# Kernel tuning notes

Measured on AMD Instinct MI355X. Metric: run time of the kernel, lower is better.

## Reference

```python
import jax, jax.numpy as jnp
import numpy as np

B, S, D = 8, 1024, 768
H, DQK, DV = 12, 64, 64
DHEAD = 2 * DQK + DV  # 192, interleaved per-head qkv layout
DOUT = 768


def setup_inputs() -> dict:
    key = jax.random.key(0)
    k1, k2, k3, k4 = jax.random.split(key, 4)
    x = jax.random.normal(k1, (B, S, D), dtype=jnp.float32)
    w_qkv = jax.random.normal(k2, (D, H * DHEAD), dtype=jnp.float32) * (D ** -0.5)
    w_out = jax.random.normal(k3, (H * DV, DOUT), dtype=jnp.float32) * ((H * DV) ** -0.5)
    b_out = jax.random.normal(k4, (DOUT,), dtype=jnp.float32) * 0.02
    return {"x": x, "w_qkv": w_qkv, "w_out": w_out, "b_out": b_out}


def reference(x, w_qkv, w_out, b_out):
    scale = DQK ** -0.5
    # Interleaved per-head layout: [B,S,H,DHEAD] then split into q|k|v blocks.
    qkv = (x @ w_qkv).reshape(B, S, H, DHEAD)
    q = qkv[..., :DQK]                 # [B,S,H,DQK]
    k = qkv[..., DQK:2 * DQK]          # [B,S,H,DQK]
    v = qkv[..., 2 * DQK:]             # [B,S,H,DV]
    scores = jnp.einsum("bshd,bthd->bhst", q, k) * scale  # [B,H,S,S]
    attn = jax.nn.softmax(scores, axis=-1)
    out = jnp.einsum("bhst,bthd->bshd", attn, v)           # [B,S,H,DV]
    out = out.reshape(B, S, H * DV)
    return out @ w_out + b_out
```

## Files before the change

kernel.cpp:

```cpp
#include <hip/hip_runtime.h>
#include <hip/hip_bf16.h>
#include <cstdint>

namespace {

constexpr int kB = 8;
constexpr int kS = 1024;
constexpr int kD = 768;
constexpr int kH = 12;
constexpr int kDH = 192;
constexpr int kNQ = kH * kDH;
constexpr int kM = kB * kS;
constexpr int kDO = 768;

using f32x4 = __attribute__((ext_vector_type(4))) float;
using s16x8 = __attribute__((ext_vector_type(8))) short;
using u16x8 = __attribute__((ext_vector_type(8))) unsigned short;

__device__ __forceinline__ unsigned short f2bf(float f) {
  union { float f; uint32_t u; } v; v.f = f;
  uint32_t u = v.u;
  u += 0x7FFFu + ((u >> 16) & 1u);
  return (unsigned short)(u >> 16);
}

__device__ __forceinline__ void load_lds16(const void* g, void* l) {
  __builtin_amdgcn_global_load_lds((__attribute__((address_space(1))) void*)g,
                                   (__attribute__((address_space(3))) void*)l,
                                   16, 0, 0);
}


__global__ __launch_bounds__(256) void cvt_x_kernel(const float* __restrict__ in,
                                                    unsigned short* __restrict__ out) {
  int i = (blockIdx.x * 256 + threadIdx.x) * 8;
  float4 a = *(const float4*)(in + i);
  float4 b = *(const float4*)(in + i + 4);
  u16x8 o;
  o[0] = f2bf(a.x); o[1] = f2bf(a.y); o[2] = f2bf(a.z); o[3] = f2bf(a.w);
  o[4] = f2bf(b.x); o[5] = f2bf(b.y); o[6] = f2bf(b.z); o[7] = f2bf(b.w);
  *(u16x8*)(out + i) = o;
}

__global__ __launch_bounds__(256) void cvt_transpose_kernel(const float* __restrict__ w,
                                                            unsigned short* __restrict__ wt,
                                                            int K, int N) {
  __shared__ float tile[32][33];
  int k0 = blockIdx.x * 32, n0 = blockIdx.y * 32;
  int tx = threadIdx.x & 31, ty = threadIdx.x >> 5;
  #pragma unroll
  for (int r = 0; r < 32; r += 8)
    tile[ty + r][tx] = w[(size_t)(k0 + ty + r) * N + n0 + tx];
  __syncthreads();
  #pragma unroll
  for (int r = 0; r < 32; r += 8)
    wt[(size_t)(n0 + ty + r) * K + k0 + tx] = f2bf(tile[tx][ty + r]);
}

template <int MODE>
__global__ __launch_bounds__(256, 2) void gemm_bt_kernel(
    const unsigned short* __restrict__ A,
    const unsigned short* __restrict__ Bt,
    void* __restrict__ Cout,
    const float* __restrict__ bias,
    int M, int N, int K) {
  __shared__ alignas(16) unsigned short Al[128 * 64];
  __shared__ alignas(16) unsigned short Bl[128 * 64];
  const int nT = N >> 7;
  const int tm = blockIdx.x / nT, tn = blockIdx.x % nT;
  const int tid = threadIdx.x;
  const int w = tid >> 6, l = tid & 63;
  const int wr = w >> 1, wc = w & 1;
  const int la = l & 15, g = l >> 4;
  const int sr = l >> 3, sc = l & 7;

  f32x4 acc[4][4] = {};
  const unsigned short* Ag = A + (size_t)(tm * 128) * K;
  const unsigned short* Bg = Bt + (size_t)(tn * 128) * K;

  for (int k0 = 0; k0 < K; k0 += 64) {
    #pragma unroll
    for (int j = 0; j < 4; ++j) {
      int row = w * 32 + j * 8 + sr;
      load_lds16(Ag + (size_t)row * K + k0 + sc * 8, &Al[row * 64 + sc * 8]);
      load_lds16(Bg + (size_t)row * K + k0 + sc * 8, &Bl[row * 64 + sc * 8]);
    }
    __syncthreads();
    #pragma unroll
    for (int kk = 0; kk < 2; ++kk) {
      s16x8 af[4], bfv[4];
      #pragma unroll
      for (int i = 0; i < 4; ++i)
        af[i] = *(const s16x8*)&Al[(wr * 64 + i * 16 + la) * 64 + kk * 32 + g * 8];
      #pragma unroll
      for (int j = 0; j < 4; ++j)
        bfv[j] = *(const s16x8*)&Bl[(wc * 64 + j * 16 + la) * 64 + kk * 32 + g * 8];
      #pragma unroll
      for (int i = 0; i < 4; ++i)
        #pragma unroll
        for (int j = 0; j < 4; ++j)
          acc[i][j] = __builtin_amdgcn_mfma_f32_16x16x32_bf16(af[i], bfv[j], acc[i][j], 0, 0, 0);
    }
    __syncthreads();
  }

  #pragma unroll
  for (int i = 0; i < 4; ++i) {
    int row0 = tm * 128 + wr * 64 + i * 16 + g * 4;
    #pragma unroll
    for (int j = 0; j < 4; ++j) {
      int col = tn * 128 + wc * 64 + j * 16 + la;
      if (MODE == 0) {
        unsigned short* C = (unsigned short*)Cout;
        float sc2 = ((col % 192) < 64) ? 0.125f : 1.0f;
        #pragma unroll
        for (int r = 0; r < 4; ++r)
          C[(size_t)(row0 + r) * N + col] = f2bf(acc[i][j][r] * sc2);
      } else {
        float* C = (float*)Cout;
        float bv = bias[col];
        #pragma unroll
        for (int r = 0; r < 4; ++r)
          C[(size_t)(row0 + r) * N + col] = acc[i][j][r] + bv;
      }
    }
  }
}

__global__ __launch_bounds__(256, 2) void attn_kernel(
    const unsigned short* __restrict__ qkv,
    unsigned short* __restrict__ Ab) {
  const int qb = blockIdx.x, h = blockIdx.y, b = blockIdx.z;
  const int tid = threadIdx.x;
  const int w = tid >> 6, l = tid & 63;
  const int la = l & 15, g = l >> 4;

  __shared__ alignas(16) unsigned short Ql[64 * 64];
  __shared__ alignas(16) unsigned short Kl[64 * 64];
  __shared__ alignas(16) unsigned short Vt[64 * 64];
  __shared__ alignas(16) unsigned short Pl[64 * 64];

  const size_t base_bs = (size_t)b * kS;
  const size_t qrow0 = base_bs + (size_t)qb * 64;

  {
    int row = tid >> 2, c0 = (tid & 3) * 2;
    const unsigned short* src = qkv + (qrow0 + row) * kNQ + h * kDH + c0 * 8;
    u16x8 v0 = *(const u16x8*)(src);
    u16x8 v1 = *(const u16x8*)(src + 8);
    int x = row & 7;
    *(u16x8*)&Ql[row * 64 + ((c0 ^ x) * 8)] = v0;
    *(u16x8*)&Ql[row * 64 + (((c0 + 1) ^ x) * 8)] = v1;
  }
  s16x8 qf[2];
  {
    int row = w * 16 + la, x = row & 7;
    #pragma unroll
    for (int ks = 0; ks < 2; ++ks)
      qf[ks] = *(const s16x8*)&Ql[row * 64 + (((ks * 4 + g) ^ x) * 8)];
  }

  float mrow[4], lrow[4];
  #pragma unroll
  for (int r = 0; r < 4; ++r) { mrow[r] = -1e30f; lrow[r] = 0.f; }
  f32x4 oacc[4] = {};
  const float LOG2E = 1.44269504088896340736f;

  for (int kt = 0; kt < 16; ++kt) {
    __syncthreads();
    {
      int row = tid >> 2, c0 = (tid & 3) * 2;
      const unsigned short* srcK = qkv + (base_bs + kt * 64 + row) * kNQ + h * kDH + 64 + c0 * 8;
      u16x8 k0v = *(const u16x8*)(srcK);
      u16x8 k1v = *(const u16x8*)(srcK + 8);
      int x = row & 7;
      *(u16x8*)&Kl[row * 64 + ((c0 ^ x) * 8)] = k0v;
      *(u16x8*)&Kl[row * 64 + (((c0 + 1) ^ x) * 8)] = k1v;

      int tv = tid >> 2, d0 = (tid & 3) * 16;
      const unsigned short* srcV = qkv + (base_bs + kt * 64 + tv) * kNQ + h * kDH + 128 + d0;
      u16x8 v0 = *(const u16x8*)(srcV);
      u16x8 v1 = *(const u16x8*)(srcV + 8);
      #pragma unroll
      for (int e = 0; e < 8; ++e) {
        int d1 = d0 + e;
        int x1 = (d1 & 7) ^ ((d1 >> 3) & 7);
        Vt[d1 * 64 + (tv ^ (x1 << 3))] = (unsigned short)v0[e];
        int d2 = d0 + 8 + e;
        int x2 = (d2 & 7) ^ ((d2 >> 3) & 7);
        Vt[d2 * 64 + (tv ^ (x2 << 3))] = (unsigned short)v1[e];
      }
    }
    __syncthreads();

    f32x4 sacc[4] = {};
    #pragma unroll
    for (int ks = 0; ks < 2; ++ks) {
      #pragma unroll
      for (int tb = 0; tb < 4; ++tb) {
        int row = tb * 16 + la, x = row & 7;
        s16x8 kf = *(const s16x8*)&Kl[row * 64 + (((ks * 4 + g) ^ x) * 8)];
        sacc[tb] = __builtin_amdgcn_mfma_f32_16x16x32_bf16(qf[ks], kf, sacc[tb], 0, 0, 0);
      }
    }

    #pragma unroll
    for (int r = 0; r < 4; ++r) {
      float m = fmaxf(fmaxf(sacc[0][r], sacc[1][r]), fmaxf(sacc[2][r], sacc[3][r]));
      #pragma unroll
      for (int msk = 1; msk < 16; msk <<= 1) m = fmaxf(m, __shfl_xor(m, msk, 64));
      float mnew = fmaxf(mrow[r], m);
      float corr = exp2f((mrow[r] - mnew) * LOG2E);
      mrow[r] = mnew;
      float s = 0.f;
      #pragma unroll
      for (int tb = 0; tb < 4; ++tb) {
        float p = exp2f((sacc[tb][r] - mnew) * LOG2E);
        sacc[tb][r] = p;
        s += p;
      }
      #pragma unroll
      for (int msk = 1; msk < 16; msk <<= 1) s += __shfl_xor(s, msk, 64);
      lrow[r] = lrow[r] * corr + s;
      #pragma unroll
      for (int db = 0; db < 4; ++db) oacc[db][r] *= corr;
    }

    #pragma unroll
    for (int r = 0; r < 4; ++r) {
      int prow = w * 16 + g * 4 + r, x = prow & 7;
      #pragma unroll
      for (int tb = 0; tb < 4; ++tb) {
        int col = tb * 16 + la;
        Pl[prow * 64 + (col ^ (x << 3))] = f2bf(sacc[tb][r]);
      }
    }

    #pragma unroll
    for (int ks = 0; ks < 2; ++ks) {
      int prow = w * 16 + la, x = prow & 7;
      s16x8 pf = *(const s16x8*)&Pl[prow * 64 + (((ks * 4 + g) ^ x) * 8)];
      #pragma unroll
      for (int db = 0; db < 4; ++db) {
        int drow = db * 16 + la;
        int xv = (drow & 7) ^ ((drow >> 3) & 7);
        s16x8 vf = *(const s16x8*)&Vt[drow * 64 + (((ks * 4 + g) ^ xv) * 8)];
        oacc[db] = __builtin_amdgcn_mfma_f32_16x16x32_bf16(pf, vf, oacc[db], 0, 0, 0);
      }
    }
  }

  #pragma unroll
  for (int db = 0; db < 4; ++db) {
    #pragma unroll
    for (int r = 0; r < 4; ++r) {
      int row = w * 16 + g * 4 + r;
      Ab[(qrow0 + row) * (size_t)(kH * 64) + h * 64 + db * 16 + la] =
          f2bf(oacc[db][r] / lrow[r]);
    }
  }
}

}

extern "C" void kernel_launch(void* const* d_in, const int* in_sizes, int n_in,
                              void* d_out, int out_size, void* d_ws, size_t ws_size,
                              hipStream_t stream) {
  (void)in_sizes; (void)n_in; (void)out_size; (void)ws_size;
  const float* x = (const float*)d_in[0];
  const float* w_qkv = (const float*)d_in[1];
  const float* w_out = (const float*)d_in[2];
  const float* b_out = (const float*)d_in[3];

  unsigned short* Xb = (unsigned short*)d_ws;
  unsigned short* WqT = Xb + (size_t)kM * kD;
  unsigned short* WoT = WqT + (size_t)kNQ * kD;
  unsigned short* QKV = WoT + (size_t)kDO * kDO;
  unsigned short* Ab = QKV + (size_t)kM * kNQ;

  cvt_x_kernel<<<dim3((kM * kD) / (256 * 8)), dim3(256), 0, stream>>>(x, Xb);
  cvt_transpose_kernel<<<dim3(kD / 32, kNQ / 32), dim3(256), 0, stream>>>(w_qkv, WqT, kD, kNQ);
  cvt_transpose_kernel<<<dim3(kDO / 32, kDO / 32), dim3(256), 0, stream>>>(w_out, WoT, kDO, kDO);

  gemm_bt_kernel<0><<<dim3((kM / 128) * (kNQ / 128)), dim3(256), 0, stream>>>(
      Xb, WqT, (void*)QKV, nullptr, kM, kNQ, kD);

  attn_kernel<<<dim3(kS / 64, kH, kB), dim3(256), 0, stream>>>(QKV, Ab);

  gemm_bt_kernel<1><<<dim3((kM / 128) * (kDO / 128)), dim3(256), 0, stream>>>(
      Ab, WoT, d_out, b_out, kM, kDO, kH * 64);
}
```

Before: 259.1 us.

## Emit transposed V from QKV GEMM and load K/V via direct-to-LDS copies

The QKV GEMM epilogue now splits its output into a compact Q|K buffer and a separate per-head transposed V buffer, so attention no longer transposes V element by element through LDS. The attention kernel reads Q fragments straight from global memory, which removes the Q LDS tile, and fills the K and V tiles with global_load_lds 16-byte copies into pre-swizzled addresses. The launch-bounds occupancy hint rises to 8 blocks. The cost is a strided 8-byte transposed store in the GEMM epilogue and one extra workspace buffer.

```diff
diff --git a/kernel.cpp b/kernel.cpp
--- a/kernel.cpp
+++ b/kernel.cpp
@@ -10,12 +10,14 @@
 constexpr int kH = 12;
 constexpr int kDH = 192;
 constexpr int kNQ = kH * kDH;
+constexpr int kNK = kH * 128;
 constexpr int kM = kB * kS;
 constexpr int kDO = 768;
 
 using f32x4 = __attribute__((ext_vector_type(4))) float;
 using s16x8 = __attribute__((ext_vector_type(8))) short;
 using u16x8 = __attribute__((ext_vector_type(8))) unsigned short;
+using u16x4 = __attribute__((ext_vector_type(4))) unsigned short;
 
 __device__ __forceinline__ unsigned short f2bf(float f) {
   union { float f; uint32_t u; } v; v.f = f;
@@ -62,6 +64,7 @@
     const unsigned short* __restrict__ A,
     const unsigned short* __restrict__ Bt,
     void* __restrict__ Cout,
+    unsigned short* __restrict__ Vtg,
     const float* __restrict__ bias,
     int M, int N, int K) {
   __shared__ alignas(16) unsigned short Al[128 * 64];
@@ -111,11 +114,22 @@
     for (int j = 0; j < 4; ++j) {
       int col = tn * 128 + wc * 64 + j * 16 + la;
       if (MODE == 0) {
-        unsigned short* C = (unsigned short*)Cout;
-        float sc2 = ((col % 192) < 64) ? 0.125f : 1.0f;
-        #pragma unroll
-        for (int r = 0; r < 4; ++r)
-          C[(size_t)(row0 + r) * N + col] = f2bf(acc[i][j][r] * sc2);
+        int h = col / kDH, colm = col % kDH;
+        if (colm < 128) {
+          unsigned short* C = (unsigned short*)Cout;
+          float sc2 = (colm < 64) ? 0.125f : 1.0f;
+          int ncol = h * 128 + colm;
+          #pragma unroll
+          for (int r = 0; r < 4; ++r)
+            C[(size_t)(row0 + r) * kNK + ncol] = f2bf(acc[i][j][r] * sc2);
+        } else {
+          int d = colm - 128;
+          int bb = row0 >> 10, t = row0 & 1023;
+          u16x4 pv;
+          #pragma unroll
+          for (int r = 0; r < 4; ++r) pv[r] = f2bf(acc[i][j][r]);
+          *(u16x4*)&Vtg[((size_t)(bb * kH + h) * 64 + d) * kS + t] = pv;
+        }
       } else {
         float* C = (float*)Cout;
         float bv = bias[col];
@@ -127,38 +141,35 @@
   }
 }
 
-__global__ __launch_bounds__(256, 2) void attn_kernel(
-    const unsigned short* __restrict__ qkv,
+__global__ __launch_bounds__(256, 8) void attn_kernel(
+    const unsigned short* __restrict__ qk,
+    const unsigned short* __restrict__ Vtg,
     unsigned short* __restrict__ Ab) {
   const int qb = blockIdx.x, h = blockIdx.y, b = blockIdx.z;
   const int tid = threadIdx.x;
   const int w = tid >> 6, l = tid & 63;
   const int la = l & 15, g = l >> 4;
 
-  __shared__ alignas(16) unsigned short Ql[64 * 64];
   __shared__ alignas(16) unsigned short Kl[64 * 64];
-  __shared__ alignas(16) unsigned short Vt[64 * 64];
+  __shared__ alignas(16) unsigned short Vl[64 * 64];
   __shared__ alignas(16) unsigned short Pl[64 * 64];
 
   const size_t base_bs = (size_t)b * kS;
   const size_t qrow0 = base_bs + (size_t)qb * 64;
 
-  {
-    int row = tid >> 2, c0 = (tid & 3) * 2;
-    const unsigned short* src = qkv + (qrow0 + row) * kNQ + h * kDH + c0 * 8;
-    u16x8 v0 = *(const u16x8*)(src);
-    u16x8 v1 = *(const u16x8*)(src + 8);
-    int x = row & 7;
-    *(u16x8*)&Ql[row * 64 + ((c0 ^ x) * 8)] = v0;
-    *(u16x8*)&Ql[row * 64 + (((c0 + 1) ^ x) * 8)] = v1;
-  }
   s16x8 qf[2];
   {
-    int row = w * 16 + la, x = row & 7;
-    #pragma unroll
-    for (int ks = 0; ks < 2; ++ks)
-      qf[ks] = *(const s16x8*)&Ql[row * 64 + (((ks * 4 + g) ^ x) * 8)];
-  }
+    const unsigned short* qp = qk + (qrow0 + w * 16 + la) * kNK + h * 128;
+    qf[0] = *(const s16x8*)(qp + g * 8);
+    qf[1] = *(const s16x8*)(qp + 32 + g * 8);
+  }
+
+  const int c0 = w * 64 + l;
+  const int c1 = 256 + w * 64 + l;
+  const int r0 = c0 >> 3, cc0 = (c0 & 7) ^ (r0 & 7);
+  const int r1 = c1 >> 3, cc1 = (c1 & 7) ^ (r1 & 7);
+  const unsigned short* Kg = qk + (base_bs)*kNK + h * 128 + 64;
+  const unsigned short* Vg = Vtg + (size_t)(b * kH + h) * 64 * kS;
 
   float mrow[4], lrow[4];
   #pragma unroll
@@ -168,29 +179,10 @@
 
   for (int kt = 0; kt < 16; ++kt) {
     __syncthreads();
-    {
-      int row = tid >> 2, c0 = (tid & 3) * 2;
-      const unsigned short* srcK = qkv + (base_bs + kt * 64 + row) * kNQ + h * kDH + 64 + c0 * 8;
-      u16x8 k0v = *(const u16x8*)(srcK);
-      u16x8 k1v = *(const u16x8*)(srcK + 8);
-      int x = row & 7;
-      *(u16x8*)&Kl[row * 64 + ((c0 ^ x) * 8)] = k0v;
-      *(u16x8*)&Kl[row * 64 + (((c0 + 1) ^ x) * 8)] = k1v;
-
-      int tv = tid >> 2, d0 = (tid & 3) * 16;
-      const unsigned short* srcV = qkv + (base_bs + kt * 64 + tv) * kNQ + h * kDH + 128 + d0;
-      u16x8 v0 = *(const u16x8*)(srcV);
-      u16x8 v1 = *(const u16x8*)(srcV + 8);
-      #pragma unroll
-      for (int e = 0; e < 8; ++e) {
-        int d1 = d0 + e;
-        int x1 = (d1 & 7) ^ ((d1 >> 3) & 7);
-        Vt[d1 * 64 + (tv ^ (x1 << 3))] = (unsigned short)v0[e];
-        int d2 = d0 + 8 + e;
-        int x2 = (d2 & 7) ^ ((d2 >> 3) & 7);
-        Vt[d2 * 64 + (tv ^ (x2 << 3))] = (unsigned short)v1[e];
-      }
-    }
+    load_lds16(Kg + (size_t)(kt * 64 + r0) * kNK + cc0 * 8, &Kl[c0 * 8]);
+    load_lds16(Kg + (size_t)(kt * 64 + r1) * kNK + cc1 * 8, &Kl[c1 * 8]);
+    load_lds16(Vg + (size_t)r0 * kS + kt * 64 + cc0 * 8, &Vl[c0 * 8]);
+    load_lds16(Vg + (size_t)r1 * kS + kt * 64 + cc1 * 8, &Vl[c1 * 8]);
     __syncthreads();
 
     f32x4 sacc[4] = {};
@@ -198,8 +190,8 @@
     for (int ks = 0; ks < 2; ++ks) {
       #pragma unroll
       for (int tb = 0; tb < 4; ++tb) {
-        int row = tb * 16 + la, x = row & 7;
-        s16x8 kf = *(const s16x8*)&Kl[row * 64 + (((ks * 4 + g) ^ x) * 8)];
+        int row = tb * 16 + la;
+        s16x8 kf = *(const s16x8*)&Kl[row * 64 + (((ks * 4 + g) ^ (row & 7)) * 8)];
         sacc[tb] = __builtin_amdgcn_mfma_f32_16x16x32_bf16(qf[ks], kf, sacc[tb], 0, 0, 0);
       }
     }
@@ -238,13 +230,12 @@
 
     #pragma unroll
     for (int ks = 0; ks < 2; ++ks) {
-      int prow = w * 16 + la, x = prow & 7;
-      s16x8 pf = *(const s16x8*)&Pl[prow * 64 + (((ks * 4 + g) ^ x) * 8)];
+      int prow = w * 16 + la;
+      s16x8 pf = *(const s16x8*)&Pl[prow * 64 + (((ks * 4 + g) ^ (prow & 7)) * 8)];
       #pragma unroll
       for (int db = 0; db < 4; ++db) {
         int drow = db * 16 + la;
-        int xv = (drow & 7) ^ ((drow >> 3) & 7);
-        s16x8 vf = *(const s16x8*)&Vt[drow * 64 + (((ks * 4 + g) ^ xv) * 8)];
+        s16x8 vf = *(const s16x8*)&Vl[drow * 64 + (((ks * 4 + g) ^ (drow & 7)) * 8)];
         oacc[db] = __builtin_amdgcn_mfma_f32_16x16x32_bf16(pf, vf, oacc[db], 0, 0, 0);
       }
     }
@@ -275,18 +266,19 @@
   unsigned short* Xb = (unsigned short*)d_ws;
   unsigned short* WqT = Xb + (size_t)kM * kD;
   unsigned short* WoT = WqT + (size_t)kNQ * kD;
-  unsigned short* QKV = WoT + (size_t)kDO * kDO;
-  unsigned short* Ab = QKV + (size_t)kM * kNQ;
+  unsigned short* QK = WoT + (size_t)kDO * kDO;
+  unsigned short* Vtg = QK + (size_t)kM * kNK;
+  unsigned short* Ab = Vtg + (size_t)kB * kH * 64 * kS;
 
   cvt_x_kernel<<<dim3((kM * kD) / (256 * 8)), dim3(256), 0, stream>>>(x, Xb);
   cvt_transpose_kernel<<<dim3(kD / 32, kNQ / 32), dim3(256), 0, stream>>>(w_qkv, WqT, kD, kNQ);
   cvt_transpose_kernel<<<dim3(kDO / 32, kDO / 32), dim3(256), 0, stream>>>(w_out, WoT, kDO, kDO);
 
   gemm_bt_kernel<0><<<dim3((kM / 128) * (kNQ / 128)), dim3(256), 0, stream>>>(
-      Xb, WqT, (void*)QKV, nullptr, kM, kNQ, kD);
-
-  attn_kernel<<<dim3(kS / 64, kH, kB), dim3(256), 0, stream>>>(QKV, Ab);
+      Xb, WqT, (void*)QK, Vtg, nullptr, kM, kNQ, kD);
+
+  attn_kernel<<<dim3(kS / 64, kH, kB), dim3(256), 0, stream>>>(QK, Vtg, Ab);
 
   gemm_bt_kernel<1><<<dim3((kM / 128) * (kDO / 128)), dim3(256), 0, stream>>>(
-      Ab, WoT, d_out, b_out, kM, kDO, kH * 64);
-}
+      Ab, WoT, d_out, nullptr, b_out, kM, kDO, kH * 64);
+}
```

Measured after the change: 252.5 us. 1.03x faster.
